# Kernel tuning notes

Hardware: AMD Instinct MI355X
Metric: run time of the kernel (lower is better)

The kernel has to match this reference:

```python
import jax, jax.numpy as jnp
import numpy as np

D = 1024
H = 16
HD = D // H
DFF = 4 * D
EPS = 1e-12


def setup_inputs() -> dict:
    key = jax.random.key(0)
    ks = jax.random.split(key, 16)
    s = lambda fan_in: 1.0 / np.sqrt(fan_in)
    inp = {
        "x": jax.random.normal(ks[0], (2, 2048, D), dtype=jnp.float32),
        "Wq": jax.random.normal(ks[1], (D, D), dtype=jnp.float32) * s(D),
        "bq": jax.random.normal(ks[2], (D,), dtype=jnp.float32) * 0.02,
        "Wk": jax.random.normal(ks[3], (D, D), dtype=jnp.float32) * s(D),
        "bk": jax.random.normal(ks[4], (D,), dtype=jnp.float32) * 0.02,
        "Wv": jax.random.normal(ks[5], (D, D), dtype=jnp.float32) * s(D),
        "bv": jax.random.normal(ks[6], (D,), dtype=jnp.float32) * 0.02,
        "Wo": jax.random.normal(ks[7], (D, D), dtype=jnp.float32) * s(D),
        "bo": jax.random.normal(ks[8], (D,), dtype=jnp.float32) * 0.02,
        "W1": jax.random.normal(ks[9], (D, DFF), dtype=jnp.float32) * s(D),
        "b1": jax.random.normal(ks[10], (DFF,), dtype=jnp.float32) * 0.02,
        "W2": jax.random.normal(ks[11], (DFF, D), dtype=jnp.float32) * s(DFF),
        "b2": jax.random.normal(ks[12], (D,), dtype=jnp.float32) * 0.02,
        "g1": jnp.ones((D,), dtype=jnp.float32),
        "s1": jnp.zeros((D,), dtype=jnp.float32),
        "g2": jnp.ones((D,), dtype=jnp.float32),
        "s2": jnp.zeros((D,), dtype=jnp.float32),
    }
    return inp


def _layer_norm(x, scale, shift):
    mean = jnp.mean(x, axis=-1, keepdims=True)
    # torch.var default is unbiased (ddof=1), matching the source module
    var = jnp.var(x, axis=-1, keepdims=True, ddof=1)
    return scale * (x - mean) / jnp.sqrt(var + EPS) + shift


def _gelu(x):
    c = jnp.sqrt(jnp.asarray(2.0 / np.pi, dtype=x.dtype))
    return 0.5 * x * (1.0 + jnp.tanh(c * (x + 0.044715 * x ** 3)))


def _block(x, Wq, bq, Wk, bk, Wv, bv, Wo, bo, W1, b1, W2, b2, g1, s1, g2, s2):
    B, S, _ = x.shape
    # pre-norm attention
    h = _layer_norm(x, g1, s1)
    q = (h @ Wq + bq).reshape(B, S, H, HD).transpose(0, 2, 1, 3)  # bhsd
    k = (h @ Wk + bk).reshape(B, S, H, HD).transpose(0, 2, 1, 3)
    v = (h @ Wv + bv).reshape(B, S, H, HD).transpose(0, 2, 1, 3)
    scores = jnp.einsum("bhqd,bhkd->bhqk", q, k)
    causal = jnp.tril(jnp.ones((S, S), dtype=bool))  # True = keep
    scores = jnp.where(causal, scores, -jnp.inf)
    attn = jax.nn.softmax(scores / np.sqrt(HD), axis=-1)
    ctx = jnp.einsum("bhqk,bhkd->bhqd", attn, v)
    ctx = ctx.transpose(0, 2, 1, 3).reshape(B, S, D)
    x = x + (ctx @ Wo + bo)
    # pre-norm MLP
    h = _layer_norm(x, g2, s2)
    h = _gelu(h @ W1 + b1) @ W2 + b2
    return x + h


def reference(x, Wq, bq, Wk, bk, Wv, bv, Wo, bo, W1, b1, W2, b2, g1, s1, g2, s2):
    return _block(x, Wq, bq, Wk, bk, Wv, bv, Wo, bo, W1, b1, W2, b2, g1, s1, g2, s2)
```

## Files before the change

### kernel.cpp

```cpp
#include <hip/hip_runtime.h>

#define D_ 1024
#define H_ 16
#define HD_ 64
#define DFF_ 4096
#define B_ 2
#define S_ 2048
#define MTOK 4096

typedef unsigned short u16;
typedef short bf16x8 __attribute__((ext_vector_type(8)));
typedef float f32x4 __attribute__((ext_vector_type(4)));

__device__ __forceinline__ u16 f2bf(float f) {
    union { float f; unsigned u; } v; v.f = f;
    return (u16)((v.u + 0x7fffu + ((v.u >> 16) & 1u)) >> 16);
}
__device__ __forceinline__ u16 f2bf_ru(float f) {
    union { float f; unsigned u; } v; v.f = f;
    return (u16)((v.u + 0x8000u) >> 16);
}

__device__ __forceinline__ void gload16(const void* g, void* l) {
    __builtin_amdgcn_global_load_lds(
        (const __attribute__((address_space(1))) unsigned int*)g,
        (__attribute__((address_space(3))) unsigned int*)l, 16, 0, 0);
}

__global__ __launch_bounds__(256) void transpose_all_kernel(
    const float* __restrict__ Wq, const float* __restrict__ Wk,
    const float* __restrict__ Wv, const float* __restrict__ Wo,
    const float* __restrict__ W1, const float* __restrict__ W2,
    u16* __restrict__ bQKV, u16* __restrict__ bWo,
    u16* __restrict__ bW1, u16* __restrict__ bW2) {
    int b = blockIdx.x;
    const float* W; u16* Wt; int K, N, nt, kt;
    if (b < 4096) {
        int w = b >> 10, t = b & 1023;
        K = 1024; N = 1024; nt = t & 31; kt = t >> 5;
        W = (w == 0) ? Wq : (w == 1) ? Wk : (w == 2) ? Wv : Wo;
        Wt = (w < 3) ? (bQKV + (size_t)w * 1048576u) : bWo;
    } else if (b < 8192) {
        int t = b - 4096;
        K = 1024; N = 4096; nt = t & 127; kt = t >> 7;
        W = W1; Wt = bW1;
    } else {
        int t = b - 8192;
        K = 4096; N = 1024; nt = t & 31; kt = t >> 5;
        W = W2; Wt = bW2;
    }
    __shared__ float tl[32][33];
    int n0 = nt * 32, k0 = kt * 32;
    int tx = threadIdx.x, ty = threadIdx.y;
#pragma unroll
    for (int i = 0; i < 4; i++)
        tl[ty + i * 8][tx] = W[(size_t)(k0 + ty + i * 8) * N + n0 + tx];
    __syncthreads();
#pragma unroll
    for (int i = 0; i < 4; i++)
        Wt[(size_t)(n0 + ty + i * 8) * K + k0 + tx] = f2bf(tl[tx][ty + i * 8]);
}

__global__ __launch_bounds__(256) void ln_kernel(
    const float* __restrict__ x, const float* __restrict__ gamma,
    const float* __restrict__ beta, u16* __restrict__ out) {
    int row = blockIdx.x, tid = threadIdx.x;
    int wave = tid >> 6, lane = tid & 63;
    const float4* xr = (const float4*)(x + (size_t)row * D_);
    float4 v = xr[tid];
    float s = v.x + v.y + v.z + v.w;
#pragma unroll
    for (int off = 1; off < 64; off <<= 1) s += __shfl_xor(s, off, 64);
    __shared__ float p1[4], p2[4];
    if (lane == 0) p1[wave] = s;
    __syncthreads();
    float mean = (p1[0] + p1[1] + p1[2] + p1[3]) * (1.0f / D_);
    float4 d = {v.x - mean, v.y - mean, v.z - mean, v.w - mean};
    float sq = d.x * d.x + d.y * d.y + d.z * d.z + d.w * d.w;
#pragma unroll
    for (int off = 1; off < 64; off <<= 1) sq += __shfl_xor(sq, off, 64);
    if (lane == 0) p2[wave] = sq;
    __syncthreads();
    float var = (p2[0] + p2[1] + p2[2] + p2[3]) * (1.0f / (D_ - 1));
    float rstd = rsqrtf(var + 1e-12f);
    float4 gv = ((const float4*)gamma)[tid];
    float4 bv = ((const float4*)beta)[tid];
    u16* orow = out + (size_t)row * D_ + tid * 4;
    orow[0] = f2bf(gv.x * d.x * rstd + bv.x);
    orow[1] = f2bf(gv.y * d.y * rstd + bv.y);
    orow[2] = f2bf(gv.z * d.z * rstd + bv.z);
    orow[3] = f2bf(gv.w * d.w * rstd + bv.w);
}

constexpr int EPI_QKV = 0, EPI_O = 3, EPI_G = 4, EPI_R = 5;

template <int EPI>
__device__ __forceinline__ void epi_store(
    float accv, int m, int n, const float* bias, const float* bias2,
    const float* bias3, const float* resid, void* Cout) {
    if constexpr (EPI == EPI_QKV) {
        int which = n >> 10, d = n & 1023;
        const float* bp = (which == 0) ? bias : (which == 1) ? bias2 : bias3;
        float cval = accv + bp[d];
        int b = m >> 11, s = m & 2047, h = d >> 6, hd = d & 63;
        u16* qkv = (u16*)Cout;
        if (which == 0)
            qkv[((size_t)(b * H_ + h) * S_ + s) * HD_ + hd] = f2bf(cval);
        else if (which == 1)
            qkv[4194304u + ((size_t)(b * H_ + h) * S_ + s) * HD_ + hd] = f2bf(cval);
        else
            qkv[8388608u + ((size_t)(b * H_ + h) * HD_ + hd) * S_ + s] = f2bf(cval);
    } else if constexpr (EPI == EPI_O) {
        float cval = accv + bias[n];
        ((float*)Cout)[(size_t)m * D_ + n] = resid[(size_t)m * D_ + n] + cval;
    } else if constexpr (EPI == EPI_G) {
        float cval = accv + bias[n];
        float u = 0.7978845608028654f * (cval + 0.044715f * cval * cval * cval);
        float t = 1.0f - 2.0f / (__expf(2.0f * u) + 1.0f);
        ((u16*)Cout)[(size_t)m * DFF_ + n] = f2bf(0.5f * cval * (1.0f + t));
    } else {
        float cval = accv + bias[n];
        ((float*)Cout)[(size_t)m * D_ + n] = resid[(size_t)m * D_ + n] + cval;
    }
}

template <int EPI, int KD, int GYB>
__global__ __launch_bounds__(256, 2) void gemm_fat_kernel(
    const u16* __restrict__ A, const u16* __restrict__ Bt,
    const float* __restrict__ bias, const float* __restrict__ bias2,
    const float* __restrict__ bias3, const float* __restrict__ resid,
    void* __restrict__ Cout) {
    __shared__ alignas(16) char Alds[3][16384];
    __shared__ alignas(16) char Blds[3][8192];
    int tid = threadIdx.x;
    int tm = (blockIdx.x & ((1 << GYB) - 1)) * 256;
    int tn = (blockIdx.x >> GYB) * 128;
    int wave = tid >> 6, lane = tid & 63;
    int lcol = lane & 15, quad = lane >> 4;
    f32x4 acc[4][8] = {};

    int l = lane >> 3, p = lane & 7, slog = p ^ l;
    int sro = l * 2 + (slog >> 2), sch = slog & 3;
    const u16* ga = A + (size_t)(tm + wave * 64 + sro) * KD + sch * 8;
    const u16* gb = Bt + (size_t)(tn + wave * 32 + sro) * KD + sch * 8;

    auto stage = [&](int k0, int slot) {
        char* lA = Alds[slot] + wave * 4096;
        char* lB = Blds[slot] + wave * 2048;
        gload16(ga + k0, lA);
        gload16(ga + (size_t)16 * KD + k0, lA + 1024);
        gload16(ga + (size_t)32 * KD + k0, lA + 2048);
        gload16(ga + (size_t)48 * KD + k0, lA + 3072);
        gload16(gb + k0, lB);
        gload16(gb + (size_t)16 * KD + k0, lB + 1024);
    };

    constexpr int NT = KD / 32;
    stage(0, 0);
    stage(32, 1);
    int swz = (lcol >> 1) * 128 + (((((lcol & 1) << 2) | quad) ^ (lcol >> 1)) * 16);
#pragma unroll 1
    for (int kt = 0; kt < NT; kt++) {
        if (kt == NT - 1) {
            asm volatile("s_waitcnt vmcnt(0)" ::: "memory");
        } else {
            asm volatile("s_waitcnt vmcnt(6)" ::: "memory");
        }
        asm volatile("s_barrier" ::: "memory");
        if (kt + 2 < NT) stage((kt + 2) * 32, (kt + 2) % 3);
        int cur = kt % 3;
        bf16x8 af[4], bfr[8];
#pragma unroll
        for (int i = 0; i < 4; i++)
            af[i] = *(const bf16x8*)(Alds[cur] + wave * 4096 + i * 1024 + swz);
#pragma unroll
        for (int j = 0; j < 8; j++)
            bfr[j] = *(const bf16x8*)(Blds[cur] + j * 1024 + swz);
#pragma unroll
        for (int i = 0; i < 4; i++)
#pragma unroll
            for (int j = 0; j < 8; j++)
                acc[i][j] = __builtin_amdgcn_mfma_f32_16x16x32_bf16(
                    af[i], bfr[j], acc[i][j], 0, 0, 0);
    }
#pragma unroll
    for (int i = 0; i < 4; i++)
#pragma unroll
        for (int j = 0; j < 8; j++)
#pragma unroll
            for (int r = 0; r < 4; r++) {
                int m = tm + wave * 64 + i * 16 + quad * 4 + r;
                int n = tn + j * 16 + lcol;
                epi_store<EPI>(acc[i][j][r], m, n, bias, bias2, bias3, resid, Cout);
            }
}

template <int EPI, int KD, int TM, int BK, int GYB>
__global__ __launch_bounds__(256) void gemm_kernel(
    const u16* __restrict__ A, const u16* __restrict__ Bt,
    const float* __restrict__ bias, const float* __restrict__ bias2,
    const float* __restrict__ bias3, const float* __restrict__ resid,
    void* __restrict__ Cout) {
    __shared__ alignas(16) char Alds[3][TM * BK * 2];
    __shared__ alignas(16) char Blds[3][128 * BK * 2];
    int tid = threadIdx.x;
    int tm = (blockIdx.x & ((1 << GYB) - 1)) * TM;
    int tn = (blockIdx.x >> GYB) * 128;
    int wave = tid >> 6, lane = tid & 63;
    int wrow = (wave >> 1) * (TM / 2), wcol = (wave & 1) * 64;
    int lcol = lane & 15, quad = lane >> 4;
    constexpr int NI = TM / 32;
    constexpr int G = (BK == 32) ? 4 : 6;
    f32x4 acc[NI][4] = {};

    const u16 *ga, *gb;
    if constexpr (BK == 32) {
        int l = lane >> 3, p = lane & 7, slog = p ^ l;
        int sro = l * 2 + (slog >> 2), sch = slog & 3;
        ga = A + (size_t)(tm + wave * 16 + sro) * KD + sch * 8;
        gb = Bt + (size_t)(tn + wave * 16 + sro) * KD + sch * 8;
    } else {
        int g = (lane & 7) ^ (lane >> 3);
        ga = A + (size_t)(tm + wave * 16 + (lane >> 3)) * KD + g * 8;
        gb = Bt + (size_t)(tn + wave * 32 + (lane >> 3)) * KD + g * 8;
    }

    auto stage = [&](int k0, int slot) {
        if constexpr (BK == 32) {
            char* lA = Alds[slot] + wave * 1024;
            char* lB = Blds[slot] + wave * 1024;
            gload16(ga + k0, lA);
            gload16(ga + (size_t)64 * KD + k0, lA + 4096);
            gload16(gb + k0, lB);
            gload16(gb + (size_t)64 * KD + k0, lB + 4096);
        } else {
            char* lA = Alds[slot] + wave * 2048;
            gload16(ga + k0, lA);
            gload16(ga + (size_t)8 * KD + k0, lA + 1024);
            char* lB = Blds[slot] + wave * 4096;
            gload16(gb + k0, lB);
            gload16(gb + (size_t)8 * KD + k0, lB + 1024);
            gload16(gb + (size_t)16 * KD + k0, lB + 2048);
            gload16(gb + (size_t)24 * KD + k0, lB + 3072);
        }
    };

    constexpr int NT = KD / BK;
    stage(0, 0);
    stage(BK, 1);
#pragma unroll 1
    for (int kt = 0; kt < NT; kt++) {
        if (kt == NT - 1) {
            asm volatile("s_waitcnt vmcnt(0)" ::: "memory");
        } else if constexpr (G == 4) {
            asm volatile("s_waitcnt vmcnt(4)" ::: "memory");
        } else {
            asm volatile("s_waitcnt vmcnt(6)" ::: "memory");
        }
        asm volatile("s_barrier" ::: "memory");
        if (kt + 2 < NT) stage((kt + 2) * BK, (kt + 2) % 3);
        int cur = kt % 3;
        if constexpr (BK == 32) {
            int swz = (lcol >> 1) * 128 + (((((lcol & 1) << 2) | quad) ^ (lcol >> 1)) * 16);
            bf16x8 af[NI], bfr[4];
#pragma unroll
            for (int i = 0; i < NI; i++)
                af[i] = *(const bf16x8*)(Alds[cur] + wrow * 64 + i * 1024 + swz);
#pragma unroll
            for (int j = 0; j < 4; j++)
                bfr[j] = *(const bf16x8*)(Blds[cur] + wcol * 64 + j * 1024 + swz);
#pragma unroll
            for (int i = 0; i < NI; i++)
#pragma unroll
                for (int j = 0; j < 4; j++)
                    acc[i][j] = __builtin_amdgcn_mfma_f32_16x16x32_bf16(
                        af[i], bfr[j], acc[i][j], 0, 0, 0);
        } else {
            int koff0 = lcol * 128 + ((quad ^ (lcol & 7)) * 16);
            int koff1 = lcol * 128 + (((4 | quad) ^ (lcol & 7)) * 16);
            bf16x8 af0[NI], af1[NI], bf0[4], bf1[4];
#pragma unroll
            for (int i = 0; i < NI; i++) {
                af0[i] = *(const bf16x8*)(Alds[cur] + (wrow + i * 16) * 128 + koff0);
                af1[i] = *(const bf16x8*)(Alds[cur] + (wrow + i * 16) * 128 + koff1);
            }
#pragma unroll
            for (int j = 0; j < 4; j++) {
                bf0[j] = *(const bf16x8*)(Blds[cur] + (wcol + j * 16) * 128 + koff0);
                bf1[j] = *(const bf16x8*)(Blds[cur] + (wcol + j * 16) * 128 + koff1);
            }
#pragma unroll
            for (int i = 0; i < NI; i++)
#pragma unroll
                for (int j = 0; j < 4; j++)
                    acc[i][j] = __builtin_amdgcn_mfma_f32_16x16x32_bf16(
                        af0[i], bf0[j], acc[i][j], 0, 0, 0);
#pragma unroll
            for (int i = 0; i < NI; i++)
#pragma unroll
                for (int j = 0; j < 4; j++)
                    acc[i][j] = __builtin_amdgcn_mfma_f32_16x16x32_bf16(
                        af1[i], bf1[j], acc[i][j], 0, 0, 0);
        }
    }
#pragma unroll
    for (int i = 0; i < NI; i++)
#pragma unroll
        for (int j = 0; j < 4; j++)
#pragma unroll
            for (int r = 0; r < 4; r++) {
                int m = tm + wrow + i * 16 + quad * 4 + r;
                int n = tn + wcol + j * 16 + lcol;
                epi_store<EPI>(acc[i][j][r], m, n, bias, bias2, bias3, resid, Cout);
            }
}

__global__ __launch_bounds__(256) void attn_kernel(
    const u16* __restrict__ q, const u16* __restrict__ k,
    const u16* __restrict__ v, u16* __restrict__ ctx) {
    __shared__ alignas(16) u16 klds[3][64 * 64];
    __shared__ alignas(16) u16 vlds[3][64 * 64];
    __shared__ alignas(16) u16 plds[4][16 * 64];
    int tid = threadIdx.x, wave = tid >> 6, lane = tid & 63;
    int quad = lane >> 4, lcol = lane & 15;
    int bh = blockIdx.x & 31, pairi = blockIdx.x >> 5;
    const u16* qbase = q + (size_t)bh * S_ * HD_;
    const u16* kbase = k + (size_t)bh * S_ * HD_;
    const u16* vbase = v + (size_t)bh * HD_ * S_;
    int g = (lane & 7) ^ (lane >> 3);
    int srow = wave * 16 + (lane >> 3);
    const u16* kp = kbase + (size_t)srow * HD_ + g * 8;
    const u16* vp = vbase + (size_t)srow * S_ + g * 8;
    char* pbase = (char*)plds + wave * 2048;
    int koff0 = lcol * 128 + ((quad ^ (lcol & 7)) * 16);
    int koff1 = lcol * 128 + (((4 | quad) ^ (lcol & 7)) * 16);
    int b = bh >> 4, h = bh & 15;
    auto stage = [&](int kt, int slot) {
        int k0 = kt * 64;
        char* kd = (char*)klds[slot] + wave * 2048;
        char* vd = (char*)vlds[slot] + wave * 2048;
        gload16(kp + (size_t)k0 * HD_, kd);
        gload16(kp + (size_t)(k0 + 8) * HD_, kd + 1024);
        gload16(vp + k0, vd);
        gload16(vp + 8 * S_ + k0, vd + 1024);
    };
#pragma unroll 1
    for (int half = 0; half < 2; half++) {
        int qt = half ? (31 - pairi) : pairi;
        int qr = qt * 64 + wave * 16;
        bf16x8 aq0 = *(const bf16x8*)(qbase + (size_t)(qr + lcol) * HD_ + quad * 8);
        bf16x8 aq1 = *(const bf16x8*)(qbase + (size_t)(qr + lcol) * HD_ + 32 + quad * 8);
        f32x4 co[4] = {};
        float li[4] = {0.0f, 0.0f, 0.0f, 0.0f};
        __syncthreads();
        stage(0, 0);
        if (qt >= 1) stage(1, 1);
#pragma unroll 1
        for (int kt = 0; kt <= qt; kt++) {
            if (kt == qt) {
                asm volatile("s_waitcnt vmcnt(0)" ::: "memory");
            } else {
                asm volatile("s_waitcnt vmcnt(4)" ::: "memory");
            }
            asm volatile("s_barrier" ::: "memory");
            if (kt + 2 <= qt) stage(kt + 2, (kt + 2) % 3);
            const u16* kl = klds[kt % 3];
            const u16* vl = vlds[kt % 3];
            f32x4 cs[4] = {};
#pragma unroll
            for (int j = 0; j < 4; j++) {
                bf16x8 bk = *(const bf16x8*)((char*)kl + j * 2048 + koff0);
                cs[j] = __builtin_amdgcn_mfma_f32_16x16x32_bf16(aq0, bk, cs[j], 0, 0, 0);
            }
#pragma unroll
            for (int j = 0; j < 4; j++) {
                bf16x8 bk = *(const bf16x8*)((char*)kl + j * 2048 + koff1);
                cs[j] = __builtin_amdgcn_mfma_f32_16x16x32_bf16(aq1, bk, cs[j], 0, 0, 0);
            }
            bool diag = (kt == qt);
#pragma unroll
            for (int r = 0; r < 4; r++) {
                int rr = quad * 4 + r;
                float p[4], ls = 0.0f;
#pragma unroll
                for (int j = 0; j < 4; j++) {
                    float sv = cs[j][r];
                    if (diag && (j * 16 + lcol > wave * 16 + rr)) sv = -1e38f;
                    p[j] = exp2f(sv * 0.18033688011112042f);
                    ls += p[j];
                }
                li[r] += ls;
                int pr = rr * 128 + (lcol & 7) * 2;
#pragma unroll
                for (int j = 0; j < 4; j++)
                    *(u16*)(pbase + pr + (((j * 2 + (lcol >> 3)) ^ (rr & 7)) * 16)) = f2bf_ru(p[j]);
            }
            {
                bf16x8 ap0 = *(const bf16x8*)(pbase + koff0);
                bf16x8 ap1 = *(const bf16x8*)(pbase + koff1);
#pragma unroll
                for (int j = 0; j < 4; j++) {
                    bf16x8 bv0 = *(const bf16x8*)((char*)vl + j * 2048 + koff0);
                    co[j] = __builtin_amdgcn_mfma_f32_16x16x32_bf16(ap0, bv0, co[j], 0, 0, 0);
                }
#pragma unroll
                for (int j = 0; j < 4; j++) {
                    bf16x8 bv1 = *(const bf16x8*)((char*)vl + j * 2048 + koff1);
                    co[j] = __builtin_amdgcn_mfma_f32_16x16x32_bf16(ap1, bv1, co[j], 0, 0, 0);
                }
            }
        }
#pragma unroll
        for (int r = 0; r < 4; r++) {
            float l = li[r];
            l += __shfl_xor(l, 1);
            l += __shfl_xor(l, 2);
            l += __shfl_xor(l, 4);
            l += __shfl_xor(l, 8);
            float inv = 1.0f / l;
            int row = qr + quad * 4 + r;
            size_t base = ((size_t)(b * S_ + row)) * D_ + h * HD_;
#pragma unroll
            for (int j = 0; j < 4; j++)
                ctx[base + j * 16 + lcol] = f2bf(co[j][r] * inv);
        }
    }
}

extern "C" void kernel_launch(void* const* d_in, const int* in_sizes, int n_in,
                              void* d_out, int out_size, void* d_ws, size_t ws_size,
                              hipStream_t stream) {
    const float* x  = (const float*)d_in[0];
    const float* Wq = (const float*)d_in[1];
    const float* bq = (const float*)d_in[2];
    const float* Wk = (const float*)d_in[3];
    const float* bk = (const float*)d_in[4];
    const float* Wv = (const float*)d_in[5];
    const float* bv = (const float*)d_in[6];
    const float* Wo = (const float*)d_in[7];
    const float* bo = (const float*)d_in[8];
    const float* W1 = (const float*)d_in[9];
    const float* b1 = (const float*)d_in[10];
    const float* W2 = (const float*)d_in[11];
    const float* b2 = (const float*)d_in[12];
    const float* g1 = (const float*)d_in[13];
    const float* s1 = (const float*)d_in[14];
    const float* g2 = (const float*)d_in[15];
    const float* s2 = (const float*)d_in[16];

    char* ws = (char*)d_ws;
    const size_t MB = 1024 * 1024;
    u16*   bWqkv = (u16*)(ws + 0 * MB);
    u16*   bWo   = (u16*)(ws + 6 * MB);
    u16*   bW1   = (u16*)(ws + 8 * MB);
    u16*   bW2   = (u16*)(ws + 16 * MB);
    u16*   hbuf  = (u16*)(ws + 24 * MB);
    u16*   qbuf  = (u16*)(ws + 32 * MB);
    u16*   ctxb  = (u16*)(ws + 56 * MB);
    float* x1    = (float*)(ws + 64 * MB);
    u16*   ffb   = (u16*)(ws + 80 * MB);

    transpose_all_kernel<<<12288, dim3(32, 8), 0, stream>>>(
        Wq, Wk, Wv, Wo, W1, W2, bWqkv, bWo, bW1, bW2);

    ln_kernel<<<MTOK, 256, 0, stream>>>(x, g1, s1, hbuf);

    gemm_fat_kernel<EPI_QKV, D_, 4><<<384, 256, 0, stream>>>(
        hbuf, bWqkv, bq, bk, bv, nullptr, qbuf);

    attn_kernel<<<512, 256, 0, stream>>>(
        qbuf, qbuf + 4194304u, qbuf + 8388608u, ctxb);

    gemm_kernel<EPI_O, D_, 64, 64, 6><<<512, 256, 0, stream>>>(
        ctxb, bWo, bo, nullptr, nullptr, x, x1);

    ln_kernel<<<MTOK, 256, 0, stream>>>(x1, g2, s2, hbuf);

    gemm_fat_kernel<EPI_G, D_, 4><<<512, 256, 0, stream>>>(
        hbuf, bW1, b1, nullptr, nullptr, nullptr, ffb);

    gemm_kernel<EPI_R, DFF_, 64, 64, 6><<<512, 256, 0, stream>>>(
        ffb, bW2, b2, nullptr, nullptr, x1, (float*)d_out);
}
```

Before: 367.7 us.

## Use 32x32 MFMA GEMM for QKV/FFN1 and fuse first LayerNorm into prep

```diff
diff --git a/kernel.cpp b/kernel.cpp
--- a/kernel.cpp
+++ b/kernel.cpp
@@ -11,6 +11,7 @@
 typedef unsigned short u16;
 typedef short bf16x8 __attribute__((ext_vector_type(8)));
 typedef float f32x4 __attribute__((ext_vector_type(4)));
+typedef float f32x16 __attribute__((ext_vector_type(16)));
 
 __device__ __forceinline__ u16 f2bf(float f) {
     union { float f; unsigned u; } v; v.f = f;
@@ -27,13 +28,45 @@
         (__attribute__((address_space(3))) unsigned int*)l, 16, 0, 0);
 }
 
-__global__ __launch_bounds__(256) void transpose_all_kernel(
+__global__ __launch_bounds__(256) void prep_kernel(
     const float* __restrict__ Wq, const float* __restrict__ Wk,
     const float* __restrict__ Wv, const float* __restrict__ Wo,
     const float* __restrict__ W1, const float* __restrict__ W2,
     u16* __restrict__ bQKV, u16* __restrict__ bWo,
-    u16* __restrict__ bW1, u16* __restrict__ bW2) {
+    u16* __restrict__ bW1, u16* __restrict__ bW2,
+    const float* __restrict__ x, const float* __restrict__ g1,
+    const float* __restrict__ s1, u16* __restrict__ hbuf) {
     int b = blockIdx.x;
+    int tid = threadIdx.x;
+    if (b >= 12288) {
+        int row = b - 12288;
+        int wave = tid >> 6, lane = tid & 63;
+        const float4* xr = (const float4*)(x + (size_t)row * D_);
+        float4 v = xr[tid];
+        float s = v.x + v.y + v.z + v.w;
+#pragma unroll
+        for (int off = 1; off < 64; off <<= 1) s += __shfl_xor(s, off, 64);
+        __shared__ float p1[4], p2[4];
+        if (lane == 0) p1[wave] = s;
+        __syncthreads();
+        float mean = (p1[0] + p1[1] + p1[2] + p1[3]) * (1.0f / D_);
+        float4 d = {v.x - mean, v.y - mean, v.z - mean, v.w - mean};
+        float sq = d.x * d.x + d.y * d.y + d.z * d.z + d.w * d.w;
+#pragma unroll
+        for (int off = 1; off < 64; off <<= 1) sq += __shfl_xor(sq, off, 64);
+        if (lane == 0) p2[wave] = sq;
+        __syncthreads();
+        float var = (p2[0] + p2[1] + p2[2] + p2[3]) * (1.0f / (D_ - 1));
+        float rstd = rsqrtf(var + 1e-12f);
+        float4 gv = ((const float4*)g1)[tid];
+        float4 bv = ((const float4*)s1)[tid];
+        u16* orow = hbuf + (size_t)row * D_ + tid * 4;
+        orow[0] = f2bf(gv.x * d.x * rstd + bv.x);
+        orow[1] = f2bf(gv.y * d.y * rstd + bv.y);
+        orow[2] = f2bf(gv.z * d.z * rstd + bv.z);
+        orow[3] = f2bf(gv.w * d.w * rstd + bv.w);
+        return;
+    }
     const float* W; u16* Wt; int K, N, nt, kt;
     if (b < 4096) {
         int w = b >> 10, t = b & 1023;
@@ -51,7 +84,7 @@
     }
     __shared__ float tl[32][33];
     int n0 = nt * 32, k0 = kt * 32;
-    int tx = threadIdx.x, ty = threadIdx.y;
+    int tx = tid & 31, ty = tid >> 5;
 #pragma unroll
     for (int i = 0; i < 4; i++)
         tl[ty + i * 8][tx] = W[(size_t)(k0 + ty + i * 8) * N + n0 + tx];
@@ -125,40 +158,121 @@
 }
 
 template <int EPI, int KD, int GYB>
-__global__ __launch_bounds__(256, 2) void gemm_fat_kernel(
+__global__ __launch_bounds__(256) void gemm32_kernel(
     const u16* __restrict__ A, const u16* __restrict__ Bt,
     const float* __restrict__ bias, const float* __restrict__ bias2,
     const float* __restrict__ bias3, const float* __restrict__ resid,
     void* __restrict__ Cout) {
-    __shared__ alignas(16) char Alds[3][16384];
+    __shared__ alignas(16) char Alds[3][8192];
     __shared__ alignas(16) char Blds[3][8192];
     int tid = threadIdx.x;
-    int tm = (blockIdx.x & ((1 << GYB) - 1)) * 256;
+    int tm = (blockIdx.x & ((1 << GYB) - 1)) * 128;
     int tn = (blockIdx.x >> GYB) * 128;
     int wave = tid >> 6, lane = tid & 63;
-    int lcol = lane & 15, quad = lane >> 4;
-    f32x4 acc[4][8] = {};
+    int wrow = (wave >> 1) * 64, wcol = (wave & 1) * 64;
+    f32x16 acc[2][2] = {};
 
     int l = lane >> 3, p = lane & 7, slog = p ^ l;
     int sro = l * 2 + (slog >> 2), sch = slog & 3;
-    const u16* ga = A + (size_t)(tm + wave * 64 + sro) * KD + sch * 8;
-    const u16* gb = Bt + (size_t)(tn + wave * 32 + sro) * KD + sch * 8;
+    const u16* ga = A + (size_t)(tm + wave * 16 + sro) * KD + sch * 8;
+    const u16* gb = Bt + (size_t)(tn + wave * 16 + sro) * KD + sch * 8;
 
     auto stage = [&](int k0, int slot) {
-        char* lA = Alds[slot] + wave * 4096;
-        char* lB = Blds[slot] + wave * 2048;
+        char* lA = Alds[slot] + wave * 1024;
+        char* lB = Blds[slot] + wave * 1024;
         gload16(ga + k0, lA);
-        gload16(ga + (size_t)16 * KD + k0, lA + 1024);
-        gload16(ga + (size_t)32 * KD + k0, lA + 2048);
-        gload16(ga + (size_t)48 * KD + k0, lA + 3072);
+        gload16(ga + (size_t)64 * KD + k0, lA + 4096);
         gload16(gb + k0, lB);
-        gload16(gb + (size_t)16 * KD + k0, lB + 1024);
+        gload16(gb + (size_t)64 * KD + k0, lB + 4096);
     };
+
+    int sec = (lane >> 4) & 1;
+    int line = (lane & 15) >> 1;
+    int rp = (lane & 1) << 2;
+    int khl = lane >> 5;
+    auto frag_off = [&](int c) { return line * 128 + (((rp | c) ^ line) * 16); };
 
     constexpr int NT = KD / 32;
     stage(0, 0);
     stage(32, 1);
-    int swz = (lcol >> 1) * 128 + (((((lcol & 1) << 2) | quad) ^ (lcol >> 1)) * 16);
+#pragma unroll 1
+    for (int kt = 0; kt < NT; kt++) {
+        if (kt == NT - 1) {
+            asm volatile("s_waitcnt vmcnt(0)" ::: "memory");
+        } else {
+            asm volatile("s_waitcnt vmcnt(4)" ::: "memory");
+        }
+        asm volatile("s_barrier" ::: "memory");
+        if (kt + 2 < NT) stage((kt + 2) * 32, (kt + 2) % 3);
+        int cur = kt % 3;
+#pragma unroll
+        for (int h = 0; h < 2; h++) {
+            int c = 2 * h + khl;
+            bf16x8 af[2], bfr[2];
+#pragma unroll
+            for (int i = 0; i < 2; i++)
+                af[i] = *(const bf16x8*)(Alds[cur] + wrow * 64 + (i * 2 + sec) * 1024 + frag_off(c));
+#pragma unroll
+            for (int j = 0; j < 2; j++)
+                bfr[j] = *(const bf16x8*)(Blds[cur] + wcol * 64 + (j * 2 + sec) * 1024 + frag_off(c));
+#pragma unroll
+            for (int i = 0; i < 2; i++)
+#pragma unroll
+                for (int j = 0; j < 2; j++)
+                    acc[i][j] = __builtin_amdgcn_mfma_f32_32x32x16_bf16(
+                        af[i], bfr[j], acc[i][j], 0, 0, 0);
+        }
+    }
+    int ncol = lane & 31;
+    int rbase = 4 * (lane >> 5);
+#pragma unroll
+    for (int i = 0; i < 2; i++)
+#pragma unroll
+        for (int j = 0; j < 2; j++)
+#pragma unroll
+            for (int reg = 0; reg < 16; reg++) {
+                int m = tm + wrow + i * 32 + (reg & 3) + 8 * (reg >> 2) + rbase;
+                int n = tn + wcol + j * 32 + ncol;
+                epi_store<EPI>(acc[i][j][reg], m, n, bias, bias2, bias3, resid, Cout);
+            }
+}
+
+template <int EPI, int KD, int GYB>
+__global__ __launch_bounds__(256) void gemm64_kernel(
+    const u16* __restrict__ A, const u16* __restrict__ Bt,
+    const float* __restrict__ bias, const float* __restrict__ bias2,
+    const float* __restrict__ bias3, const float* __restrict__ resid,
+    void* __restrict__ Cout) {
+    __shared__ alignas(16) char Alds[3][8192];
+    __shared__ alignas(16) char Blds[3][16384];
+    int tid = threadIdx.x;
+    int tm = (blockIdx.x & ((1 << GYB) - 1)) * 64;
+    int tn = (blockIdx.x >> GYB) * 128;
+    int wave = tid >> 6, lane = tid & 63;
+    int wrow = (wave >> 1) * 32, wcol = (wave & 1) * 64;
+    int lcol = lane & 15, quad = lane >> 4;
+    f32x4 acc[2][4] = {};
+
+    int g = (lane & 7) ^ (lane >> 3);
+    const u16* ga = A + (size_t)(tm + wave * 16 + (lane >> 3)) * KD + g * 8;
+    const u16* gb = Bt + (size_t)(tn + wave * 32 + (lane >> 3)) * KD + g * 8;
+
+    auto stage = [&](int k0, int slot) {
+        char* lA = Alds[slot] + wave * 2048;
+        gload16(ga + k0, lA);
+        gload16(ga + (size_t)8 * KD + k0, lA + 1024);
+        char* lB = Blds[slot] + wave * 4096;
+        gload16(gb + k0, lB);
+        gload16(gb + (size_t)8 * KD + k0, lB + 1024);
+        gload16(gb + (size_t)16 * KD + k0, lB + 2048);
+        gload16(gb + (size_t)24 * KD + k0, lB + 3072);
+    };
+
+    constexpr int NT = KD / 64;
+    stage(0, 0);
+    stage(64, 1);
+    int koff0 = lcol * 128 + ((quad ^ (lcol & 7)) * 16);
+    int koff1 = lcol * 128 + (((4 | quad) ^ (lcol & 7)) * 16);
 #pragma unroll 1
     for (int kt = 0; kt < NT; kt++) {
         if (kt == NT - 1) {
@@ -167,144 +281,34 @@
             asm volatile("s_waitcnt vmcnt(6)" ::: "memory");
         }
         asm volatile("s_barrier" ::: "memory");
-        if (kt + 2 < NT) stage((kt + 2) * 32, (kt + 2) % 3);
+        if (kt + 2 < NT) stage((kt + 2) * 64, (kt + 2) % 3);
         int cur = kt % 3;
-        bf16x8 af[4], bfr[8];
-#pragma unroll
-        for (int i = 0; i < 4; i++)
-            af[i] = *(const bf16x8*)(Alds[cur] + wave * 4096 + i * 1024 + swz);
-#pragma unroll
-        for (int j = 0; j < 8; j++)
-            bfr[j] = *(const bf16x8*)(Blds[cur] + j * 1024 + swz);
-#pragma unroll
-        for (int i = 0; i < 4; i++)
-#pragma unroll
-            for (int j = 0; j < 8; j++)
+        bf16x8 af0[2], af1[2], bf0[4], bf1[4];
+#pragma unroll
+        for (int i = 0; i < 2; i++) {
+            af0[i] = *(const bf16x8*)(Alds[cur] + (wrow + i * 16) * 128 + koff0);
+            af1[i] = *(const bf16x8*)(Alds[cur] + (wrow + i * 16) * 128 + koff1);
+        }
+#pragma unroll
+        for (int j = 0; j < 4; j++) {
+            bf0[j] = *(const bf16x8*)(Blds[cur] + (wcol + j * 16) * 128 + koff0);
+            bf1[j] = *(const bf16x8*)(Blds[cur] + (wcol + j * 16) * 128 + koff1);
+        }
+#pragma unroll
+        for (int i = 0; i < 2; i++)
+#pragma unroll
+            for (int j = 0; j < 4; j++)
                 acc[i][j] = __builtin_amdgcn_mfma_f32_16x16x32_bf16(
-                    af[i], bfr[j], acc[i][j], 0, 0, 0);
-    }
-#pragma unroll
-    for (int i = 0; i < 4; i++)
-#pragma unroll
-        for (int j = 0; j < 8; j++)
-#pragma unroll
-            for (int r = 0; r < 4; r++) {
-                int m = tm + wave * 64 + i * 16 + quad * 4 + r;
-                int n = tn + j * 16 + lcol;
-                epi_store<EPI>(acc[i][j][r], m, n, bias, bias2, bias3, resid, Cout);
-            }
-}
-
-template <int EPI, int KD, int TM, int BK, int GYB>
-__global__ __launch_bounds__(256) void gemm_kernel(
-    const u16* __restrict__ A, const u16* __restrict__ Bt,
-    const float* __restrict__ bias, const float* __restrict__ bias2,
-    const float* __restrict__ bias3, const float* __restrict__ resid,
-    void* __restrict__ Cout) {
-    __shared__ alignas(16) char Alds[3][TM * BK * 2];
-    __shared__ alignas(16) char Blds[3][128 * BK * 2];
-    int tid = threadIdx.x;
-    int tm = (blockIdx.x & ((1 << GYB) - 1)) * TM;
-    int tn = (blockIdx.x >> GYB) * 128;
-    int wave = tid >> 6, lane = tid & 63;
-    int wrow = (wave >> 1) * (TM / 2), wcol = (wave & 1) * 64;
-    int lcol = lane & 15, quad = lane >> 4;
-    constexpr int NI = TM / 32;
-    constexpr int G = (BK == 32) ? 4 : 6;
-    f32x4 acc[NI][4] = {};
-
-    const u16 *ga, *gb;
-    if constexpr (BK == 32) {
-        int l = lane >> 3, p = lane & 7, slog = p ^ l;
-        int sro = l * 2 + (slog >> 2), sch = slog & 3;
-        ga = A + (size_t)(tm + wave * 16 + sro) * KD + sch * 8;
-        gb = Bt + (size_t)(tn + wave * 16 + sro) * KD + sch * 8;
-    } else {
-        int g = (lane & 7) ^ (lane >> 3);
-        ga = A + (size_t)(tm + wave * 16 + (lane >> 3)) * KD + g * 8;
-        gb = Bt + (size_t)(tn + wave * 32 + (lane >> 3)) * KD + g * 8;
-    }
-
-    auto stage = [&](int k0, int slot) {
-        if constexpr (BK == 32) {
-            char* lA = Alds[slot] + wave * 1024;
-            char* lB = Blds[slot] + wave * 1024;
-            gload16(ga + k0, lA);
-            gload16(ga + (size_t)64 * KD + k0, lA + 4096);
-            gload16(gb + k0, lB);
-            gload16(gb + (size_t)64 * KD + k0, lB + 4096);
-        } else {
-            char* lA = Alds[slot] + wave * 2048;
-            gload16(ga + k0, lA);
-            gload16(ga + (size_t)8 * KD + k0, lA + 1024);
-            char* lB = Blds[slot] + wave * 4096;
-            gload16(gb + k0, lB);
-            gload16(gb + (size_t)8 * KD + k0, lB + 1024);
-            gload16(gb + (size_t)16 * KD + k0, lB + 2048);
-            gload16(gb + (size_t)24 * KD + k0, lB + 3072);
-        }
-    };
-
-    constexpr int NT = KD / BK;
-    stage(0, 0);
-    stage(BK, 1);
-#pragma unroll 1
-    for (int kt = 0; kt < NT; kt++) {
-        if (kt == NT - 1) {
-            asm volatile("s_waitcnt vmcnt(0)" ::: "memory");
-        } else if constexpr (G == 4) {
-            asm volatile("s_waitcnt vmcnt(4)" ::: "memory");
-        } else {
-            asm volatile("s_waitcnt vmcnt(6)" ::: "memory");
-        }
-        asm volatile("s_barrier" ::: "memory");
-        if (kt + 2 < NT) stage((kt + 2) * BK, (kt + 2) % 3);
-        int cur = kt % 3;
-        if constexpr (BK == 32) {
-            int swz = (lcol >> 1) * 128 + (((((lcol & 1) << 2) | quad) ^ (lcol >> 1)) * 16);
-            bf16x8 af[NI], bfr[4];
-#pragma unroll
-            for (int i = 0; i < NI; i++)
-                af[i] = *(const bf16x8*)(Alds[cur] + wrow * 64 + i * 1024 + swz);
+                    af0[i], bf0[j], acc[i][j], 0, 0, 0);
+#pragma unroll
+        for (int i = 0; i < 2; i++)
 #pragma unroll
             for (int j = 0; j < 4; j++)
-                bfr[j] = *(const bf16x8*)(Blds[cur] + wcol * 64 + j * 1024 + swz);
-#pragma unroll
-            for (int i = 0; i < NI; i++)
-#pragma unroll
-                for (int j = 0; j < 4; j++)
-                    acc[i][j] = __builtin_amdgcn_mfma_f32_16x16x32_bf16(
-                        af[i], bfr[j], acc[i][j], 0, 0, 0);
-        } else {
-            int koff0 = lcol * 128 + ((quad ^ (lcol & 7)) * 16);
-            int koff1 = lcol * 128 + (((4 | quad) ^ (lcol & 7)) * 16);
-            bf16x8 af0[NI], af1[NI], bf0[4], bf1[4];
-#pragma unroll
-            for (int i = 0; i < NI; i++) {
-                af0[i] = *(const bf16x8*)(Alds[cur] + (wrow + i * 16) * 128 + koff0);
-                af1[i] = *(const bf16x8*)(Alds[cur] + (wrow + i * 16) * 128 + koff1);
-            }
-#pragma unroll
-            for (int j = 0; j < 4; j++) {
-                bf0[j] = *(const bf16x8*)(Blds[cur] + (wcol + j * 16) * 128 + koff0);
-                bf1[j] = *(const bf16x8*)(Blds[cur] + (wcol + j * 16) * 128 + koff1);
-            }
-#pragma unroll
-            for (int i = 0; i < NI; i++)
-#pragma unroll
-                for (int j = 0; j < 4; j++)
-                    acc[i][j] = __builtin_amdgcn_mfma_f32_16x16x32_bf16(
-                        af0[i], bf0[j], acc[i][j], 0, 0, 0);
-#pragma unroll
-            for (int i = 0; i < NI; i++)
-#pragma unroll
-                for (int j = 0; j < 4; j++)
-                    acc[i][j] = __builtin_amdgcn_mfma_f32_16x16x32_bf16(
-                        af1[i], bf1[j], acc[i][j], 0, 0, 0);
-        }
-    }
-#pragma unroll
-    for (int i = 0; i < NI; i++)
+                acc[i][j] = __builtin_amdgcn_mfma_f32_16x16x32_bf16(
+                    af1[i], bf1[j], acc[i][j], 0, 0, 0);
+    }
+#pragma unroll
+    for (int i = 0; i < 2; i++)
 #pragma unroll
         for (int j = 0; j < 4; j++)
 #pragma unroll
@@ -460,25 +464,23 @@
     float* x1    = (float*)(ws + 64 * MB);
     u16*   ffb   = (u16*)(ws + 80 * MB);
 
-    transpose_all_kernel<<<12288, dim3(32, 8), 0, stream>>>(
-        Wq, Wk, Wv, Wo, W1, W2, bWqkv, bWo, bW1, bW2);
-
-    ln_kernel<<<MTOK, 256, 0, stream>>>(x, g1, s1, hbuf);
-
-    gemm_fat_kernel<EPI_QKV, D_, 4><<<384, 256, 0, stream>>>(
+    prep_kernel<<<16384, 256, 0, stream>>>(
+        Wq, Wk, Wv, Wo, W1, W2, bWqkv, bWo, bW1, bW2, x, g1, s1, hbuf);
+
+    gemm32_kernel<EPI_QKV, D_, 5><<<768, 256, 0, stream>>>(
         hbuf, bWqkv, bq, bk, bv, nullptr, qbuf);
 
     attn_kernel<<<512, 256, 0, stream>>>(
         qbuf, qbuf + 4194304u, qbuf + 8388608u, ctxb);
 
-    gemm_kernel<EPI_O, D_, 64, 64, 6><<<512, 256, 0, stream>>>(
+    gemm64_kernel<EPI_O, D_, 6><<<512, 256, 0, stream>>>(
         ctxb, bWo, bo, nullptr, nullptr, x, x1);
 
     ln_kernel<<<MTOK, 256, 0, stream>>>(x1, g2, s2, hbuf);
 
-    gemm_fat_kernel<EPI_G, D_, 4><<<512, 256, 0, stream>>>(
+    gemm32_kernel<EPI_G, D_, 5><<<1024, 256, 0, stream>>>(
         hbuf, bW1, b1, nullptr, nullptr, nullptr, ffb);
 
-    gemm_kernel<EPI_R, DFF_, 64, 64, 6><<<512, 256, 0, stream>>>(
+    gemm64_kernel<EPI_R, DFF_, 6><<<512, 256, 0, stream>>>(
         ffb, bW2, b2, nullptr, nullptr, x1, (float*)d_out);
 }
```

Result: no change. 373.1 us (+1.5%).
